# Performance work log

Hardware: AMD Instinct MI355X
Metric: run time of the kernel (lower is better)

The kernel has to match this reference:

```python
import jax, jax.numpy as jnp
import numpy as np

WINDOW = 128
STRIDE = 16

def setup_inputs() -> dict:
    key = jax.random.key(0)
    input_data = jax.random.normal(key, (16, 4096, 128), dtype=jnp.float32)
    return {"input_data": input_data}

def reference(input_data) -> jnp.ndarray:
    B, T, F = input_data.shape
    num_windows = (T - WINDOW) // STRIDE + 1  # 249
    # time indices for every window: [num_windows, WINDOW]
    idx = jnp.arange(num_windows)[:, None] * STRIDE + jnp.arange(WINDOW)[None, :]
    # gather overlapping windows: [B, num_windows, WINDOW, F]
    windows = input_data[:, idx, :]
    # per-window X^T X / WINDOW: [B, num_windows, F, F]
    pccs = jnp.einsum('bwlf,bwlg->bwfg', windows, windows) / WINDOW
    return pccs
```

## Files before the change

kernel.cpp:

```cpp
#include <hip/hip_runtime.h>

#define WINDOW 128
#define STRIDE 16
#define NWIN   249
#define NF     128
#define SEQ    4096

typedef _Float16 f16x8 __attribute__((ext_vector_type(8)));
typedef float    f32x4 __attribute__((ext_vector_type(4)));

__global__ __launch_bounds__(256) void pcc_kernel(const float* __restrict__ in,
                                                  float* __restrict__ out) {
    __shared__ _Float16 lds[NF * WINDOW];

    const int tid = threadIdx.x;
    const int w = blockIdx.x;
    const int b = blockIdx.y;

    const float* src = in + ((size_t)b * SEQ + (size_t)w * STRIDE) * NF;

    {
        const int f0 = 4 * (tid & 31);
        const int lb = 8 * (tid >> 5);
        #pragma unroll
        for (int pass = 0; pass < 2; ++pass) {
            const int l0 = pass * 64 + lb;
            f32x4 rows[8];
            #pragma unroll
            for (int j = 0; j < 8; ++j)
                rows[j] = *(const f32x4*)&src[(size_t)(l0 + j) * NF + f0];
            #pragma unroll
            for (int d = 0; d < 4; ++d) {
                const int f = f0 + d;
                f16x8 v;
                #pragma unroll
                for (int j = 0; j < 8; ++j)
                    v[j] = (_Float16)rows[j][d];
                const int chunk = (l0 >> 3) ^ (f & 15);
                *(f16x8*)&lds[f * WINDOW + (chunk << 3)] = v;
            }
        }
    }
    __syncthreads();

    const int lane = tid & 63;
    const int wid  = tid >> 6;
    const int q    = lane >> 4;
    const int c    = lane & 15;

    f32x4 acc[2][8];
    #pragma unroll
    for (int i = 0; i < 2; ++i)
        #pragma unroll
        for (int t = 0; t < 8; ++t)
            acc[i][t] = f32x4{0.f, 0.f, 0.f, 0.f};

    #pragma unroll
    for (int ks = 0; ks < 4; ++ks) {
        const int chunk = ((4 * ks + q) ^ c) << 3;
        f16x8 bfrag[8];
        #pragma unroll
        for (int t = 0; t < 8; ++t)
            bfrag[t] = *(const f16x8*)&lds[(16 * t + c) * WINDOW + chunk];
        f16x8 afrag0 = *(const f16x8*)&lds[(16 * (2 * wid + 0) + c) * WINDOW + chunk];
        f16x8 afrag1 = *(const f16x8*)&lds[(16 * (2 * wid + 1) + c) * WINDOW + chunk];
        #pragma unroll
        for (int t = 0; t < 8; ++t) {
            acc[0][t] = __builtin_amdgcn_mfma_f32_16x16x32_f16(afrag0, bfrag[t], acc[0][t], 0, 0, 0);
            acc[1][t] = __builtin_amdgcn_mfma_f32_16x16x32_f16(afrag1, bfrag[t], acc[1][t], 0, 0, 0);
        }
    }

    float* dst = out + (size_t)(b * NWIN + w) * (NF * NF);
    const float scale = 1.0f / (float)WINDOW;
    #pragma unroll
    for (int i = 0; i < 2; ++i) {
        const int rowbase = 16 * (2 * wid + i) + 4 * q;
        #pragma unroll
        for (int t = 0; t < 8; ++t) {
            #pragma unroll
            for (int r = 0; r < 4; ++r) {
                const int row = rowbase + r;
                const int col = 16 * t + c;
                dst[row * NF + col] = acc[i][t][r] * scale;
            }
        }
    }
}

extern "C" void kernel_launch(void* const* d_in, const int* in_sizes, int n_in,
                              void* d_out, int out_size, void* d_ws, size_t ws_size,
                              hipStream_t stream) {
    (void)in_sizes; (void)n_in; (void)d_ws; (void)ws_size; (void)out_size;
    const float* in = (const float*)d_in[0];
    float* out = (float*)d_out;
    dim3 grid(NWIN, 16);
    pcc_kernel<<<grid, dim3(256, 1, 1), 0, stream>>>(in, out);
}
```

Before: 317.9 us.

## Compute two overlapping windows per block from one shared staged tile

Each block now stages 160 time rows (covering two adjacent windows at stride 16) into LDS once and computes both windows' Gram matrices from it, halving the grid. The last block handles only the final window. It also folds the 1/WINDOW scaling into the fp16 conversion by multiplying by 1/sqrt(128), and uses packed round-toward-zero conversion. This cuts redundant global loads and conversion work. The cost is a larger LDS footprint and more serial MFMA work per block, and the pre-scaling slightly changes fp16 rounding.

```diff
diff --git a/kernel.cpp b/kernel.cpp
--- a/kernel.cpp
+++ b/kernel.cpp
@@ -5,49 +5,41 @@
 #define NWIN   249
 #define NF     128
 #define SEQ    4096
+#define LROWS  160
 
+typedef _Float16 f16;
+typedef _Float16 f16x2 __attribute__((ext_vector_type(2)));
 typedef _Float16 f16x8 __attribute__((ext_vector_type(8)));
 typedef float    f32x4 __attribute__((ext_vector_type(4)));
 
-__global__ __launch_bounds__(256) void pcc_kernel(const float* __restrict__ in,
-                                                  float* __restrict__ out) {
-    __shared__ _Float16 lds[NF * WINDOW];
+union V8 { f16x8 v8; f16x2 v2[4]; };
 
-    const int tid = threadIdx.x;
-    const int w = blockIdx.x;
-    const int b = blockIdx.y;
+__device__ __forceinline__ void stage8(const float* __restrict__ src, f16* lds,
+                                       int f0, int l0) {
+    f32x4 rows[8];
+    #pragma unroll
+    for (int j = 0; j < 8; ++j)
+        rows[j] = *(const f32x4*)&src[(size_t)(l0 + j) * NF + f0];
+    const int cbase = l0 >> 3;
+    #pragma unroll
+    for (int d = 0; d < 4; ++d) {
+        const int f = f0 + d;
+        V8 u;
+        #pragma unroll
+        for (int jj = 0; jj < 4; ++jj) {
+            auto p = __builtin_amdgcn_cvt_pkrtz(rows[2 * jj][d], rows[2 * jj + 1][d]);
+            u.v2[jj] = *(f16x2*)&p;
+        }
+        u.v8 = u.v8 * (f16)0.08838834764831845f;
+        const int ch = (l0 < 128) ? (cbase ^ (f & 15))
+                                  : (16 + ((cbase & 3) ^ (f & 3)));
+        *(f16x8*)&lds[f * LROWS + ch * 8] = u.v8;
+    }
+}
 
-    const float* src = in + ((size_t)b * SEQ + (size_t)w * STRIDE) * NF;
-
-    {
-        const int f0 = 4 * (tid & 31);
-        const int lb = 8 * (tid >> 5);
-        #pragma unroll
-        for (int pass = 0; pass < 2; ++pass) {
-            const int l0 = pass * 64 + lb;
-            f32x4 rows[8];
-            #pragma unroll
-            for (int j = 0; j < 8; ++j)
-                rows[j] = *(const f32x4*)&src[(size_t)(l0 + j) * NF + f0];
-            #pragma unroll
-            for (int d = 0; d < 4; ++d) {
-                const int f = f0 + d;
-                f16x8 v;
-                #pragma unroll
-                for (int j = 0; j < 8; ++j)
-                    v[j] = (_Float16)rows[j][d];
-                const int chunk = (l0 >> 3) ^ (f & 15);
-                *(f16x8*)&lds[f * WINDOW + (chunk << 3)] = v;
-            }
-        }
-    }
-    __syncthreads();
-
-    const int lane = tid & 63;
-    const int wid  = tid >> 6;
-    const int q    = lane >> 4;
-    const int c    = lane & 15;
-
+template<int CO>
+__device__ __forceinline__ void compute_and_store(const f16* lds, int c, int q,
+                                                  int wid, float* __restrict__ dst) {
     f32x4 acc[2][8];
     #pragma unroll
     for (int i = 0; i < 2; ++i)
@@ -57,35 +49,66 @@
 
     #pragma unroll
     for (int ks = 0; ks < 4; ++ks) {
-        const int chunk = ((4 * ks + q) ^ c) << 3;
+        const int clog = CO + 4 * ks + q;
+        int pc;
+        if (CO == 0) pc = clog ^ c;
+        else pc = (clog < 16) ? (clog ^ c) : (16 + ((clog & 3) ^ (c & 3)));
+        const int off = pc * 8;
+
         f16x8 bfrag[8];
         #pragma unroll
         for (int t = 0; t < 8; ++t)
-            bfrag[t] = *(const f16x8*)&lds[(16 * t + c) * WINDOW + chunk];
-        f16x8 afrag0 = *(const f16x8*)&lds[(16 * (2 * wid + 0) + c) * WINDOW + chunk];
-        f16x8 afrag1 = *(const f16x8*)&lds[(16 * (2 * wid + 1) + c) * WINDOW + chunk];
+            bfrag[t] = *(const f16x8*)&lds[(16 * t + c) * LROWS + off];
+        const f16x8 a0 = *(const f16x8*)&lds[(16 * (2 * wid + 0) + c) * LROWS + off];
+        const f16x8 a1 = *(const f16x8*)&lds[(16 * (2 * wid + 1) + c) * LROWS + off];
         #pragma unroll
         for (int t = 0; t < 8; ++t) {
-            acc[0][t] = __builtin_amdgcn_mfma_f32_16x16x32_f16(afrag0, bfrag[t], acc[0][t], 0, 0, 0);
-            acc[1][t] = __builtin_amdgcn_mfma_f32_16x16x32_f16(afrag1, bfrag[t], acc[1][t], 0, 0, 0);
+            acc[0][t] = __builtin_amdgcn_mfma_f32_16x16x32_f16(a0, bfrag[t], acc[0][t], 0, 0, 0);
+            acc[1][t] = __builtin_amdgcn_mfma_f32_16x16x32_f16(a1, bfrag[t], acc[1][t], 0, 0, 0);
         }
     }
 
-    float* dst = out + (size_t)(b * NWIN + w) * (NF * NF);
-    const float scale = 1.0f / (float)WINDOW;
     #pragma unroll
     for (int i = 0; i < 2; ++i) {
         const int rowbase = 16 * (2 * wid + i) + 4 * q;
         #pragma unroll
-        for (int t = 0; t < 8; ++t) {
+        for (int t = 0; t < 8; ++t)
             #pragma unroll
-            for (int r = 0; r < 4; ++r) {
-                const int row = rowbase + r;
-                const int col = 16 * t + c;
-                dst[row * NF + col] = acc[i][t][r] * scale;
-            }
-        }
+            for (int r = 0; r < 4; ++r)
+                dst[(rowbase + r) * NF + 16 * t + c] = acc[i][t][r];
     }
+}
+
+__global__ __launch_bounds__(256) void pcc_kernel(const float* __restrict__ in,
+                                                  float* __restrict__ out) {
+    __shared__ f16 lds[NF * LROWS];
+
+    const int tid = threadIdx.x;
+    const int wp  = blockIdx.x;
+    const int b   = blockIdx.y;
+    const bool full = (wp < 124);
+    const int stage_base = full ? 32 * wp : (SEQ - 144);
+
+    const float* src = in + ((size_t)b * SEQ + stage_base) * NF;
+    const int f0 = 4 * (tid & 31);
+    const int lh = tid >> 5;
+
+    stage8(src, lds, f0, 8 * lh);
+    stage8(src, lds, f0, 64 + 8 * lh);
+    if (tid < 64)
+        stage8(src, lds, f0, 128 + 8 * lh);
+    __syncthreads();
+
+    const int lane = tid & 63;
+    const int wid  = tid >> 6;
+    const int q    = lane >> 4;
+    const int c    = lane & 15;
+
+    float* outb = out + (size_t)b * NWIN * (NF * NF);
+    if (full)
+        compute_and_store<0>(lds, c, q, wid, outb + (size_t)(2 * wp) * (NF * NF));
+    const int w1 = full ? (2 * wp + 1) : (NWIN - 1);
+    compute_and_store<2>(lds, c, q, wid, outb + (size_t)w1 * (NF * NF));
 }
 
 extern "C" void kernel_launch(void* const* d_in, const int* in_sizes, int n_in,
@@ -94,6 +117,6 @@
     (void)in_sizes; (void)n_in; (void)d_ws; (void)ws_size; (void)out_size;
     const float* in = (const float*)d_in[0];
     float* out = (float*)d_out;
-    dim3 grid(NWIN, 16);
+    dim3 grid(125, 16);
     pcc_kernel<<<grid, dim3(256, 1, 1), 0, stream>>>(in, out);
 }
```

Result: faster. 295.6 us (-7.0%).
